# Kernel tuning notes

Hardware: AMD Instinct MI355X
Metric: run time of the kernel (lower is better)

## Reference

```python
import jax, jax.numpy as jnp
import numpy as np

N_ATOMS = 50000
N_NBRS = 32
R_CUTOFF = 5.0
N_BASIS = 128
N_FILTERS = 128
N_GAUSS = 25
MAX_Z = 100
MEAN = 0.0
STDDEV = 20.0


def ssp(x):
    # shifted softplus: softplus(x) - log(2)
    return jax.nn.softplus(x) - jnp.log(2.0)


def setup_inputs() -> dict:
    key = jax.random.key(0)
    ks = jax.random.split(key, 18)
    dR = jax.random.uniform(ks[0], (N_ATOMS, N_NBRS), dtype=jnp.float32) * R_CUTOFF
    Z = jax.random.randint(ks[1], (N_ATOMS,), 0, MAX_Z)
    nbr_idx = jax.random.randint(ks[2], (N_ATOMS, N_NBRS), 0, N_ATOMS)

    def p(k, shape):
        fan_in = shape[0]
        return (jax.random.normal(k, shape, dtype=jnp.float32) / np.sqrt(fan_in)).astype(jnp.float32)

    return dict(
        dR=dR, Z=Z, nbr_idx=nbr_idx,
        embed_table=jax.random.normal(ks[3], (MAX_Z, N_BASIS), dtype=jnp.float32),
        fw1=p(ks[4], (N_GAUSS, N_FILTERS)), fb1=jnp.zeros((N_FILTERS,), jnp.float32),
        fw2=p(ks[5], (N_FILTERS, N_FILTERS)), fb2=jnp.zeros((N_FILTERS,), jnp.float32),
        in2f_w=p(ks[6], (N_BASIS, N_FILTERS)),
        f2out_w1=p(ks[7], (N_FILTERS, N_BASIS)), f2out_b1=jnp.zeros((N_BASIS,), jnp.float32),
        f2out_w2=p(ks[8], (N_BASIS, N_BASIS)), f2out_b2=jnp.zeros((N_BASIS,), jnp.float32),
        mlp_w1=p(ks[9], (N_BASIS, 64)), mlp_b1=jnp.zeros((64,), jnp.float32),
        mlp_w2=p(ks[10], (64, 1)), mlp_b2=jnp.zeros((1,), jnp.float32),
    )


def reference(dR, Z, nbr_idx, embed_table, fw1, fb1, fw2, fb2, in2f_w,
              f2out_w1, f2out_b1, f2out_w2, f2out_b2,
              mlp_w1, mlp_b1, mlp_w2, mlp_b2):
    # embedding lookup: [N, B]
    x = embed_table[Z]

    # gaussian smearing of distances: [N, K, G]
    offsets = jnp.linspace(0.0, R_CUTOFF, N_GAUSS, dtype=jnp.float32)
    coeff = -0.5 / (offsets[1] - offsets[0]) ** 2
    dr_exp = jnp.exp(coeff * (dR[..., None] - offsets) ** 2)

    # filter network: Dense+ssp, Dense -> [N, K, F]
    W = ssp(jnp.einsum('nkg,gf->nkf', dr_exp, fw1) + fb1)
    W = jnp.einsum('nkf,fh->nkh', W, fw2) + fb2

    # cosine cutoff
    fcut = 0.5 * (jnp.cos(dR * jnp.pi / R_CUTOFF) + 1.0) * (dR < R_CUTOFF)
    W = W * fcut[..., None]

    # cfconv: in2f (no bias), neighbor gather, elementwise filter, sum over neighbors
    y = x @ in2f_w                    # [N, F]
    y_nbrs = y[nbr_idx]               # [N, K, F] irregular gather
    mask = (nbr_idx < N_ATOMS)[..., None]
    agg = jnp.sum(jnp.where(mask, y_nbrs * W, 0.0), axis=1)  # [N, F]

    # f2out: Dense+ssp, Dense
    v = ssp(agg @ f2out_w1 + f2out_b1) @ f2out_w2 + f2out_b2

    # residual update
    x = x + v

    # atomwise MLP [128 -> 64 -> 1] with ssp between layers
    yi = ssp(x @ mlp_w1 + mlp_b1) @ mlp_w2 + mlp_b2  # [N, 1]
    yi = yi * STDDEV + MEAN

    # aggregate (sum over atom axis), per_atom=False
    return jnp.sum(yi, axis=0)  # [1]
```

## Files before the change

kernel.cpp:

```cpp
#include <hip/hip_runtime.h>
#include <math.h>

#define N_ATOMS  50000
#define N_NBRS   32
#define N_GAUSS  25
#define RCUT     5.0f
#define TT       192
#define TROWS    32
#define NTB      6
#define MAXZ     100
#define NT32     1563
#define PBLOCKS  256
#define PI_F     3.14159265358979323846f

typedef unsigned int   uint_t;
typedef unsigned short ushort_t;
typedef _Float16 f16;
typedef f16   f16x2 __attribute__((ext_vector_type(2)));
typedef f16   f16x4 __attribute__((ext_vector_type(4)));
typedef f16   f16x8 __attribute__((ext_vector_type(8)));
typedef float f32x4 __attribute__((ext_vector_type(4)));

__device__ __forceinline__ float ssp(float x) {
  return fmaxf(x, 0.0f) + __logf(fmaf(0.5f, __expf(-fabsf(x)), 0.5f));
}
__device__ __forceinline__ f16x2 bch(uint_t u) {
  return __builtin_bit_cast(f16x2, u);
}
__device__ __forceinline__ uint_t hcb(f16x2 v) {
  return __builtin_bit_cast(uint_t, v);
}
__device__ __forceinline__ int swz(int m, int e) {
  return m * 128 + ((((e >> 3) ^ m) & 15) << 3) + (e & 7);
}

__global__ void __launch_bounds__(256, 2)
prep_all_kernel(const float* __restrict__ fw1,
                const float* __restrict__ fb1,
                const float* __restrict__ fw2,
                const float* __restrict__ fb2,
                const float* __restrict__ w1,
                const float* __restrict__ w2,
                const float* __restrict__ mw1,
                const float* __restrict__ embed,
                const float* __restrict__ in2f,
                f16* __restrict__ tabh,
                f16* __restrict__ ytab,
                f16* __restrict__ w1ht,
                f16* __restrict__ w2ht,
                f16* __restrict__ mw1ht) {
  const int tid = threadIdx.x;
  const int bid = blockIdx.x;

  __shared__ float sW2[128 * 128];
  __shared__ float sH[TROWS][128];

  if (bid < NTB) {
    const int i0 = bid * TROWS;
    #pragma unroll
    for (int t = 0; t < 16; ++t) {
      const int e = tid + t * 256;
      ((float4*)sW2)[e] = ((const float4*)fw2)[e];
    }
    {
      const int f  = tid & 127;
      const int rh = (tid >> 7) * (TROWS / 2);
      const float delta = RCUT / (float)(N_GAUSS - 1);
      const float coeff = -0.5f / (delta * delta);
      const float b1v = fb1[f];
      for (int j = 0; j < TROWS / 2; ++j) {
        const float r = (float)(i0 + rh + j) * (RCUT / 191.0f);
        float h = b1v;
        #pragma unroll
        for (int g = 0; g < N_GAUSS; ++g) {
          const float d = r - (float)g * delta;
          h = fmaf(__expf(coeff * d * d), fw1[g * 128 + f], h);
        }
        sH[rh + j][f] = ssp(h);
      }
    }
    __syncthreads();
    {
      const int c0 = (tid & 31) * 4;
      const int rg = (tid >> 5) * 4;
      f32x4 acc[4];
      const float4 bv = *(const float4*)&fb2[c0];
      #pragma unroll
      for (int j = 0; j < 4; ++j) acc[j] = (f32x4){bv.x, bv.y, bv.z, bv.w};
      for (int k = 0; k < 128; ++k) {
        const float4 wv = *(const float4*)&sW2[k * 128 + c0];
        #pragma unroll
        for (int j = 0; j < 4; ++j) {
          const float hv = sH[rg + j][k];
          acc[j][0] = fmaf(hv, wv.x, acc[j][0]);
          acc[j][1] = fmaf(hv, wv.y, acc[j][1]);
          acc[j][2] = fmaf(hv, wv.z, acc[j][2]);
          acc[j][3] = fmaf(hv, wv.w, acc[j][3]);
        }
      }
      #pragma unroll
      for (int j = 0; j < 4; ++j) {
        const int i = i0 + rg + j;
        const float r = (float)i * (RCUT / 191.0f);
        const float fc = (r < RCUT) ? 0.5f * (__cosf(r * PI_F / RCUT) + 1.0f) : 0.0f;
        f16x4 o;
        #pragma unroll
        for (int c = 0; c < 4; ++c) o[c] = (f16)(acc[j][c] * fc);
        *(f16x4*)&tabh[i * 128 + c0] = o;
      }
    }
  } else {
    const int cc = (bid - NTB) * 2 + (tid >> 7);
    const int i  = tid & 127;
    w1ht[cc * 128 + i] = (f16)w1[i * 128 + cc];
    w2ht[cc * 128 + i] = (f16)w2[i * 128 + cc];
    if (cc < 64) mw1ht[cc * 128 + i] = (f16)mw1[i * 64 + cc];
    float* xs = &sH[0][0] + (tid >> 7) * 128;
    xs[i] = (cc < MAXZ) ? embed[cc * 128 + i] : 0.0f;
    __syncthreads();
    if (cc < MAXZ) {
      float acc = 0.0f;
      for (int j = 0; j < 128; j += 4) {
        const float4 xv = *reinterpret_cast<const float4*>(&xs[j]);
        acc = fmaf(xv.x, in2f[(j + 0) * 128 + i], acc);
        acc = fmaf(xv.y, in2f[(j + 1) * 128 + i], acc);
        acc = fmaf(xv.z, in2f[(j + 2) * 128 + i], acc);
        acc = fmaf(xv.w, in2f[(j + 3) * 128 + i], acc);
      }
      ytab[cc * 128 + i] = (f16)acc;
    }
  }
}

__global__ void __launch_bounds__(512, 2)
fused_kernel(const float* __restrict__ dR,
             const int* __restrict__ Z,
             const int* __restrict__ nbr,
             const float* __restrict__ embed,
             const f16* __restrict__ tabh,
             const f16* __restrict__ ytab,
             const f16* __restrict__ w1ht, const float* __restrict__ b1,
             const f16* __restrict__ w2ht, const float* __restrict__ b2,
             const f16* __restrict__ mw1ht, const float* __restrict__ mb1,
             const float* __restrict__ mw2,
             float* __restrict__ partial) {
  const int tid = threadIdx.x;
  const int w   = tid >> 6;
  const int l   = tid & 63;
  const int q   = l >> 4;
  const int cq  = l & 15;
  const int bid = blockIdx.x;

  __shared__ __align__(16) f16    sW[TT * 128];
  __shared__ __align__(16) f16    sYT[MAXZ * 128];
  __shared__ __align__(16) uint_t s_pk[2][1024];
  __shared__ __align__(16) f16    aggB[2][32 * 128];
  __shared__ __align__(16) f16    sB[32 * 128];
  __shared__ __align__(16) f16    sX[32 * 128];
  __shared__ int   sZb[2][32];
  __shared__ float sRed[8];

  for (int e = tid; e < TT * 16; e += 512)   ((uint4*)sW)[e]  = ((const uint4*)tabh)[e];
  for (int e = tid; e < MAXZ * 16; e += 512) ((uint4*)sYT)[e] = ((const uint4*)ytab)[e];

  const int g   = w >> 2;
  const int wvg = w & 3;
  const int rc  = cq;
  const int qk  = q;
  f16x8 bw1[2][4], bw2[2][4], bwm[4];
  float bb1[2], bb2[2];
  #pragma unroll
  for (int t = 0; t < 2; ++t) {
    const int c = wvg * 32 + t * 16 + rc;
    bb1[t] = b1[c];
    bb2[t] = b2[c];
    #pragma unroll
    for (int k0i = 0; k0i < 4; ++k0i) {
      bw1[t][k0i] = *(const f16x8*)&w1ht[c * 128 + k0i * 32 + qk * 8];
      bw2[t][k0i] = *(const f16x8*)&w2ht[c * 128 + k0i * 32 + qk * 8];
    }
  }
  const int c1 = wvg * 16 + rc;
  #pragma unroll
  for (int k0i = 0; k0i < 4; ++k0i)
    bwm[k0i] = *(const f16x8*)&mw1ht[c1 * 128 + k0i * 32 + qk * 8];
  const float bm = mb1[c1];
  const float cm = mw2[c1];

  const int m = w * 4 + q;
  const char* wb = (const char*)sW  + cq * 16;
  const char* yb = (const char*)sYT + cq * 16;

  const int myChunks = (NT32 - 1 - bid) / PBLOCKS + 1;
  float vsum = 0.0f;

  f16x2 acc[4];
  uint4 twA[4], ytA[4], twB[4], ytB[4];

#define STAGE(bb, cc) { \
    const int a0s = (cc) * 32; \
    _Pragma("unroll") \
    for (int t0 = 0; t0 < 2; ++t0) { \
      const int t = tid + t0 * 512; \
      const int pidx = a0s * N_NBRS + t; \
      uint_t pk = 0; \
      if (pidx < N_ATOMS * N_NBRS) { \
        const float r = dR[pidx]; \
        const int nb = nbr[pidx]; \
        int i0 = (int)(r * (191.0f / RCUT) + 0.5f); \
        i0 = min(i0, 191); \
        pk = (uint_t)i0 | ((uint_t)Z[nb] << 8); \
      } \
      s_pk[bb][t] = pk; \
    } \
    if (tid < 32) sZb[bb][tid] = (a0s + tid < N_ATOMS) ? Z[a0s + tid] : 0; }

#define IG(BK, bb, gi) { \
    _Pragma("unroll") \
    for (int d = 0; d < 4; ++d) { \
      const uint_t pk = s_pk[bb][m * N_NBRS + (gi) * 4 + d]; \
      tw##BK[d] = *(const uint4*)(wb + ((pk & 0xFFu) << 8)); \
      yt##BK[d] = *(const uint4*)(yb + ((pk >> 8) << 8)); \
    } }

#define CG(BK) { \
    _Pragma("unroll") \
    for (int d = 0; d < 4; ++d) { \
      acc[0] += bch(tw##BK[d].x) * bch(yt##BK[d].x); \
      acc[1] += bch(tw##BK[d].y) * bch(yt##BK[d].y); \
      acc[2] += bch(tw##BK[d].z) * bch(yt##BK[d].z); \
      acc[3] += bch(tw##BK[d].w) * bch(yt##BK[d].w); \
    } }

#define AGGW(bb) { \
    uint4 o; \
    o.x = hcb(acc[0]); o.y = hcb(acc[1]); o.z = hcb(acc[2]); o.w = hcb(acc[3]); \
    const int mm = m & 15; \
    *(uint4*)&aggB[bb][(m >> 4) * 2048 + mm * 128 + (((cq ^ mm) & 15) << 3)] = o; }

#define AFRAGP(P, k0) (*(const f16x8*)&(P)[rc * 128 + (((((k0) >> 3) + qk) ^ rc) & 15) * 8])

  STAGE(0, bid)
  __syncthreads();
  #pragma unroll
  for (int c = 0; c < 4; ++c) acc[c] = (f16x2)0;
  IG(A, 0, 0) IG(B, 0, 1)
  CG(A) IG(A, 0, 2)
  CG(B) IG(B, 0, 3)
  CG(A) IG(A, 0, 4)
  CG(B) IG(B, 0, 5)
  CG(A) IG(A, 0, 6)
  CG(B) IG(B, 0, 7)
  CG(A)
  CG(B)
  AGGW(0)
  __syncthreads();

  for (int s = 0; s < myChunks; ++s) {
    const int b  = s & 1;
    const int cc = bid + s * PBLOCKS;
    const bool hn = (s + 1 < myChunks);
    const int nb_ = b ^ 1;

    if (hn) STAGE(nb_, cc + PBLOCKS)
    __syncthreads();

    if (hn) {
      #pragma unroll
      for (int c = 0; c < 4; ++c) acc[c] = (f16x2)0;
    }

    if (hn) { IG(A, nb_, 0) IG(B, nb_, 1) }
    {
      const f16* aggp = &aggB[b][g * 2048];
      f32x4 dacc[2];
      #pragma unroll
      for (int t = 0; t < 2; ++t) dacc[t] = (f32x4){bb1[t], bb1[t], bb1[t], bb1[t]};
      #pragma unroll
      for (int k0i = 0; k0i < 4; ++k0i) {
        const f16x8 af = AFRAGP(aggp, k0i * 32);
        #pragma unroll
        for (int t = 0; t < 2; ++t)
          dacc[t] = __builtin_amdgcn_mfma_f32_16x16x32_f16(af, bw1[t][k0i], dacc[t], 0, 0, 0);
      }
      f16* hB = &sB[g * 2048];
      #pragma unroll
      for (int t = 0; t < 2; ++t) {
        const int c = wvg * 32 + t * 16 + rc;
        #pragma unroll
        for (int r = 0; r < 4; ++r) hB[swz(qk * 4 + r, c)] = (f16)ssp(dacc[t][r]);
      }
    }
    if (hn) { CG(A) IG(A, nb_, 2) CG(B) CG(A) }
    __syncthreads();

    if (hn) { IG(A, nb_, 3) IG(B, nb_, 4) }
    {
      const f16* hB = &sB[g * 2048];
      f16* hX = &sX[g * 2048];
      f32x4 dacc[2];
      #pragma unroll
      for (int t = 0; t < 2; ++t) dacc[t] = (f32x4){bb2[t], bb2[t], bb2[t], bb2[t]};
      #pragma unroll
      for (int k0i = 0; k0i < 4; ++k0i) {
        const f16x8 af = AFRAGP(hB, k0i * 32);
        #pragma unroll
        for (int t = 0; t < 2; ++t)
          dacc[t] = __builtin_amdgcn_mfma_f32_16x16x32_f16(af, bw2[t][k0i], dacc[t], 0, 0, 0);
      }
      #pragma unroll
      for (int t = 0; t < 2; ++t) {
        const int c = wvg * 32 + t * 16 + rc;
        #pragma unroll
        for (int r = 0; r < 4; ++r) {
          const int mm = qk * 4 + r;
          const float x = embed[(size_t)sZb[b][g * 16 + mm] * 128 + c] + dacc[t][r];
          hX[swz(mm, c)] = (f16)x;
        }
      }
    }
    if (hn) { CG(A) IG(A, nb_, 5) CG(B) CG(A) }
    __syncthreads();

    if (hn) { IG(A, nb_, 6) IG(B, nb_, 7) }
    {
      const f16* hX = &sX[g * 2048];
      f32x4 a2 = (f32x4){bm, bm, bm, bm};
      #pragma unroll
      for (int k0i = 0; k0i < 4; ++k0i)
        a2 = __builtin_amdgcn_mfma_f32_16x16x32_f16(AFRAGP(hX, k0i * 32), bwm[k0i], a2, 0, 0, 0);
      #pragma unroll
      for (int r = 0; r < 4; ++r) {
        const int atom = cc * 32 + g * 16 + qk * 4 + r;
        if (atom < N_ATOMS) vsum = fmaf(ssp(a2[r]), cm, vsum);
      }
    }
    if (hn) { CG(A) CG(B) AGGW(nb_) }
    __syncthreads();
  }
#undef STAGE
#undef IG
#undef CG
#undef AGGW
#undef AFRAGP

  #pragma unroll
  for (int o = 1; o < 64; o <<= 1) vsum += __shfl_xor(vsum, o, 64);
  if (l == 0) sRed[w] = vsum;
  __syncthreads();
  if (tid == 0) {
    float sF = 0.0f;
    #pragma unroll
    for (int i = 0; i < 8; ++i) sF += sRed[i];
    partial[bid] = sF;
  }
}

__global__ void __launch_bounds__(256, 1)
reduce_kernel(const float* __restrict__ partial,
              const float* __restrict__ mb2,
              float* __restrict__ out) {
  const int tid = threadIdx.x;
  float s = 0.0f;
  for (int i = tid; i < PBLOCKS; i += 256) s += partial[i];
  __shared__ float sr[4];
  #pragma unroll
  for (int o = 1; o < 64; o <<= 1) s += __shfl_xor(s, o, 64);
  if ((tid & 63) == 0) sr[tid >> 6] = s;
  __syncthreads();
  if (tid == 0) {
    out[0] = 20.0f * (sr[0] + sr[1] + sr[2] + sr[3] + (float)N_ATOMS * mb2[0]);
  }
}

extern "C" void kernel_launch(void* const* d_in, const int* in_sizes, int n_in,
                              void* d_out, int out_size, void* d_ws, size_t ws_size,
                              hipStream_t stream) {
  const float* dR    = (const float*)d_in[0];
  const int*   Z     = (const int*)  d_in[1];
  const int*   nbr   = (const int*)  d_in[2];
  const float* embed = (const float*)d_in[3];
  const float* fw1   = (const float*)d_in[4];
  const float* fb1   = (const float*)d_in[5];
  const float* fw2   = (const float*)d_in[6];
  const float* fb2   = (const float*)d_in[7];
  const float* in2f  = (const float*)d_in[8];
  const float* w1    = (const float*)d_in[9];
  const float* b1    = (const float*)d_in[10];
  const float* w2    = (const float*)d_in[11];
  const float* b2    = (const float*)d_in[12];
  const float* mw1   = (const float*)d_in[13];
  const float* mb1   = (const float*)d_in[14];
  const float* mw2   = (const float*)d_in[15];
  const float* mb2   = (const float*)d_in[16];
  float* out = (float*)d_out;

  char* ws = (char*)d_ws;
  f16*   tabh    = (f16*)ws;
  f16*   ytab    = (f16*)(ws + (size_t)64 * 1024);
  f16*   w1ht    = (f16*)(ws + (size_t)128 * 1024);
  f16*   w2ht    = (f16*)(ws + (size_t)192 * 1024);
  f16*   mw1ht   = (f16*)(ws + (size_t)256 * 1024);
  float* partial = (float*)(ws + (size_t)384 * 1024);

  prep_all_kernel<<<NTB + 64, 256, 0, stream>>>(fw1, fb1, fw2, fb2,
      w1, w2, mw1, embed, in2f, tabh, ytab, w1ht, w2ht, mw1ht);
  fused_kernel<<<PBLOCKS, 512, 0, stream>>>(dR, Z, nbr, embed,
      tabh, ytab, w1ht, b1, w2ht, b2, mw1ht, mb1, mw2, partial);
  reduce_kernel<<<1, 256, 0, stream>>>(partial, mb2, out);
}
```

Baseline: 57.24 us.

## Precompute packed neighbor keys in prep kernel and prefetch two chunks ahead

Moves the per-pair quantization of distances and the gather of neighbor Z values into extra blocks of the prep kernel, which writes a packed uint array to workspace. The fused kernel's staging step becomes a single coalesced 8-byte load per thread. Staging is now issued two chunks ahead, placed after the IG of the current stage, which removes one __syncthreads per iteration. The cost is an extra ~6.4MB write and read through global memory plus more prep-kernel blocks.

```diff
diff --git a/kernel.cpp b/kernel.cpp
--- a/kernel.cpp
+++ b/kernel.cpp
@@ -11,6 +11,9 @@
 #define MAXZ     100
 #define NT32     1563
 #define PBLOCKS  256
+#define NPAIR    (N_ATOMS * N_NBRS)
+#define PKPAD    (NT32 * 1024)
+#define PKB      782
 #define PI_F     3.14159265358979323846f
 
 typedef unsigned int   uint_t;
@@ -44,16 +47,40 @@
                 const float* __restrict__ mw1,
                 const float* __restrict__ embed,
                 const float* __restrict__ in2f,
+                const float* __restrict__ dR,
+                const int* __restrict__ nbr,
+                const int* __restrict__ Z,
                 f16* __restrict__ tabh,
                 f16* __restrict__ ytab,
                 f16* __restrict__ w1ht,
                 f16* __restrict__ w2ht,
-                f16* __restrict__ mw1ht) {
+                f16* __restrict__ mw1ht,
+                uint_t* __restrict__ pkAll) {
   const int tid = threadIdx.x;
   const int bid = blockIdx.x;
 
   __shared__ float sW2[128 * 128];
   __shared__ float sH[TROWS][128];
+
+  if (bid >= NTB + 64) {
+    const int base = (bid - NTB - 64) * 2048;
+    #pragma unroll
+    for (int t0 = 0; t0 < 8; ++t0) {
+      const int idx = base + t0 * 256 + tid;
+      if (idx < PKPAD) {
+        uint_t pk = 0;
+        if (idx < NPAIR) {
+          const float r = dR[idx];
+          const int  nb = nbr[idx];
+          int i0 = (int)(r * (191.0f / RCUT) + 0.5f);
+          i0 = min(i0, 191);
+          pk = (uint_t)i0 | ((uint_t)Z[nb] << 8);
+        }
+        pkAll[idx] = pk;
+      }
+    }
+    return;
+  }
 
   if (bid < NTB) {
     const int i0 = bid * TROWS;
@@ -133,9 +160,8 @@
 }
 
 __global__ void __launch_bounds__(512, 2)
-fused_kernel(const float* __restrict__ dR,
+fused_kernel(const uint_t* __restrict__ pkAll,
              const int* __restrict__ Z,
-             const int* __restrict__ nbr,
              const float* __restrict__ embed,
              const f16* __restrict__ tabh,
              const f16* __restrict__ ytab,
@@ -198,22 +224,9 @@
   uint4 twA[4], ytA[4], twB[4], ytB[4];
 
 #define STAGE(bb, cc) { \
-    const int a0s = (cc) * 32; \
-    _Pragma("unroll") \
-    for (int t0 = 0; t0 < 2; ++t0) { \
-      const int t = tid + t0 * 512; \
-      const int pidx = a0s * N_NBRS + t; \
-      uint_t pk = 0; \
-      if (pidx < N_ATOMS * N_NBRS) { \
-        const float r = dR[pidx]; \
-        const int nb = nbr[pidx]; \
-        int i0 = (int)(r * (191.0f / RCUT) + 0.5f); \
-        i0 = min(i0, 191); \
-        pk = (uint_t)i0 | ((uint_t)Z[nb] << 8); \
-      } \
-      s_pk[bb][t] = pk; \
-    } \
-    if (tid < 32) sZb[bb][tid] = (a0s + tid < N_ATOMS) ? Z[a0s + tid] : 0; }
+    const uint2 v = *(const uint2*)&pkAll[(cc) * 1024 + tid * 2]; \
+    *(uint2*)&s_pk[bb][tid * 2] = v; \
+    if (tid < 32) sZb[bb][tid] = ((cc) * 32 + tid < N_ATOMS) ? Z[(cc) * 32 + tid] : 0; }
 
 #define IG(BK, bb, gi) { \
     _Pragma("unroll") \
@@ -241,6 +254,7 @@
 #define AFRAGP(P, k0) (*(const f16x8*)&(P)[rc * 128 + (((((k0) >> 3) + qk) ^ rc) & 15) * 8])
 
   STAGE(0, bid)
+  if (1 < myChunks) STAGE(1, bid + PBLOCKS)
   __syncthreads();
   #pragma unroll
   for (int c = 0; c < 4; ++c) acc[c] = (f16x2)0;
@@ -262,9 +276,6 @@
     const bool hn = (s + 1 < myChunks);
     const int nb_ = b ^ 1;
 
-    if (hn) STAGE(nb_, cc + PBLOCKS)
-    __syncthreads();
-
     if (hn) {
       #pragma unroll
       for (int c = 0; c < 4; ++c) acc[c] = (f16x2)0;
@@ -323,6 +334,7 @@
     __syncthreads();
 
     if (hn) { IG(A, nb_, 6) IG(B, nb_, 7) }
+    if (s + 2 < myChunks) STAGE(b, bid + (s + 2) * PBLOCKS)
     {
       const f16* hX = &sX[g * 2048];
       f32x4 a2 = (f32x4){bm, bm, bm, bm};
@@ -396,16 +408,18 @@
   float* out = (float*)d_out;
 
   char* ws = (char*)d_ws;
-  f16*   tabh    = (f16*)ws;
-  f16*   ytab    = (f16*)(ws + (size_t)64 * 1024);
-  f16*   w1ht    = (f16*)(ws + (size_t)128 * 1024);
-  f16*   w2ht    = (f16*)(ws + (size_t)192 * 1024);
-  f16*   mw1ht   = (f16*)(ws + (size_t)256 * 1024);
-  float* partial = (float*)(ws + (size_t)384 * 1024);
-
-  prep_all_kernel<<<NTB + 64, 256, 0, stream>>>(fw1, fb1, fw2, fb2,
-      w1, w2, mw1, embed, in2f, tabh, ytab, w1ht, w2ht, mw1ht);
-  fused_kernel<<<PBLOCKS, 512, 0, stream>>>(dR, Z, nbr, embed,
+  f16*    tabh    = (f16*)ws;
+  f16*    ytab    = (f16*)(ws + (size_t)64 * 1024);
+  f16*    w1ht    = (f16*)(ws + (size_t)128 * 1024);
+  f16*    w2ht    = (f16*)(ws + (size_t)192 * 1024);
+  f16*    mw1ht   = (f16*)(ws + (size_t)256 * 1024);
+  float*  partial = (float*)(ws + (size_t)384 * 1024);
+  uint_t* pkAll   = (uint_t*)(ws + (size_t)1024 * 1024);
+
+  prep_all_kernel<<<NTB + 64 + PKB, 256, 0, stream>>>(fw1, fb1, fw2, fb2,
+      w1, w2, mw1, embed, in2f, dR, nbr, Z,
+      tabh, ytab, w1ht, w2ht, mw1ht, pkAll);
+  fused_kernel<<<PBLOCKS, 512, 0, stream>>>(pkAll, Z, embed,
       tabh, ytab, w1ht, b1, w2ht, b2, mw1ht, mb1, mw2, partial);
   reduce_kernel<<<1, 256, 0, stream>>>(partial, mb2, out);
 }
```

Measured after the change: 53.38 us. 6.7% less time.
